# Kernel tuning notes

Hardware: AMD Instinct MI355X
Metric: run time of the kernel (lower is better)

Reference implementation:

```python
import jax, jax.numpy as jnp
import numpy as np

N, S, D, H = 4, 2048, 1024, 16
DH = D // H  # 64


def setup_inputs() -> dict:
    key = jax.random.key(0)
    ks = jax.random.split(key, 7)
    return {
        "sequences": jax.random.normal(ks[0], (N, S, D), dtype=jnp.float32),
        "Wq": jax.random.normal(ks[1], (H, DH, DH), dtype=jnp.float32) * (1.0 / np.sqrt(DH)),
        "bq": jax.random.normal(ks[2], (H, DH), dtype=jnp.float32) * 0.02,
        "Wk": jax.random.normal(ks[3], (H, DH, DH), dtype=jnp.float32) * (1.0 / np.sqrt(DH)),
        "bk": jax.random.normal(ks[4], (H, DH), dtype=jnp.float32) * 0.02,
        "Wv": jax.random.normal(ks[5], (H, DH, DH), dtype=jnp.float32) * (1.0 / np.sqrt(DH)),
        "bv": jax.random.normal(ks[6], (H, DH), dtype=jnp.float32) * 0.02,
    }


def reference(sequences, Wq, bq, Wk, bk, Wv, bv):
    n, s, d = sequences.shape
    # Each head h only sees its own slice of the embedding (block-diagonal proj)
    x = sequences.reshape(n, s, H, DH)  # (N, S, H, DH)
    q = jnp.einsum('nshd,hde->nshe', x, Wq) + bq  # (N, S, H, DH)
    k = jnp.einsum('nshd,hde->nshe', x, Wk) + bk
    v = jnp.einsum('nshd,hde->nshe', x, Wv) + bv
    scores = jnp.einsum('nqhd,nkhd->nhqk', q, k) / jnp.sqrt(jnp.float32(DH))
    attn = jax.nn.softmax(scores, axis=-1)  # (N, H, S, S)
    out = jnp.einsum('nhqk,nkhd->nqhd', attn, v)  # (N, S, H, DH)
    return out.reshape(n, s, d)  # hstack of heads == concat on last dim
```

## Files before the change

kernel.cpp:

```cpp
#include <hip/hip_runtime.h>
#include <hip/hip_bf16.h>

#define NB 4
#define SLEN 2048
#define DMODEL 1024
#define NH 16
#define DH 64

using f32x4  = __attribute__((ext_vector_type(4))) float;
using f32x8  = __attribute__((ext_vector_type(8))) float;
using f32x16 = __attribute__((ext_vector_type(16))) float;
using bf16x8 = __attribute__((ext_vector_type(8))) short;
using u32x4  = __attribute__((ext_vector_type(4))) unsigned int;

__device__ __forceinline__ unsigned short f2bf(float f) {
    unsigned int u = __float_as_uint(f);
    u += 0x7FFFu + ((u >> 16) & 1u);
    return (unsigned short)(u >> 16);
}

__device__ __forceinline__ float fast_exp2(float x) {
    float r;
    asm("v_exp_f32 %0, %1" : "=v"(r) : "v"(x));
    return r;
}

__device__ __forceinline__ unsigned cvtpk(float lo, float hi) {
    unsigned r;
    asm("v_cvt_pk_bf16_f32 %0, %1, %2" : "=v"(r) : "v"(lo), "v"(hi));
    return r;
}

__device__ __forceinline__ void permswap(unsigned& a, unsigned& b) {
    asm("v_permlane32_swap_b32 %0, %1" : "+v"(a), "+v"(b));
}

#define QSCALE 0.18033688011112042f

__global__ __launch_bounds__(256) void qkv_proj_kernel(
    const float* __restrict__ seq,
    const float* __restrict__ Wq, const float* __restrict__ bq,
    const float* __restrict__ Wk, const float* __restrict__ bk,
    const float* __restrict__ Wv, const float* __restrict__ bv,
    unsigned short* __restrict__ Qb,
    unsigned short* __restrict__ Kb,
    unsigned short* __restrict__ Vt)
{
    const int bid  = blockIdx.x;
    const int nh   = bid >> 5;
    const int tile = bid & 31;
    const int h = nh & 15;
    const int n = nh >> 4;
    const int t0 = tile * 64;
    const int tid = threadIdx.x;
    const int w  = tid >> 6;
    const int l  = tid & 63;
    const int g  = l >> 4;
    const int ln = l & 15;

    __shared__ unsigned short wt[3][64 * 72];

    {
        const float* Wsrc0 = Wq + h * 4096;
        const float* Wsrc1 = Wk + h * 4096;
        const float* Wsrc2 = Wv + h * 4096;
        for (int idx = tid; idx < 4096; idx += 256) {
            int d = idx >> 6, e = idx & 63;
            wt[0][e * 72 + d] = f2bf(Wsrc0[idx]);
            wt[1][e * 72 + d] = f2bf(Wsrc1[idx]);
            wt[2][e * 72 + d] = f2bf(Wsrc2[idx]);
        }
    }
    __syncthreads();

    const float* xrow = seq + ((size_t)(n * SLEN + t0 + w * 16 + ln)) * DMODEL + h * DH;
    bf16x8 a[2];
#pragma unroll
    for (int kk = 0; kk < 2; ++kk) {
        const float4* src = reinterpret_cast<const float4*>(xrow + kk * 32 + g * 8);
        float4 v0 = src[0];
        float4 v1 = src[1];
        bf16x8 av;
        av[0] = (short)f2bf(v0.x); av[1] = (short)f2bf(v0.y);
        av[2] = (short)f2bf(v0.z); av[3] = (short)f2bf(v0.w);
        av[4] = (short)f2bf(v1.x); av[5] = (short)f2bf(v1.y);
        av[6] = (short)f2bf(v1.z); av[7] = (short)f2bf(v1.w);
        a[kk] = av;
    }

    const float* bias0 = bq + h * DH;
    const float* bias1 = bk + h * DH;
    const float* bias2 = bv + h * DH;

#pragma unroll
    for (int p = 0; p < 3; ++p) {
#pragma unroll
        for (int cb = 0; cb < 4; ++cb) {
            f32x4 acc = {0.f, 0.f, 0.f, 0.f};
#pragma unroll
            for (int kk = 0; kk < 2; ++kk) {
                bf16x8 b = *reinterpret_cast<bf16x8*>(
                    &wt[p][(cb * 16 + ln) * 72 + kk * 32 + g * 8]);
                acc = __builtin_amdgcn_mfma_f32_16x16x32_bf16(a[kk], b, acc, 0, 0, 0);
            }
            const int col = cb * 16 + ln;
            if (p == 0) {
                const float bb = bias0[col];
#pragma unroll
                for (int r = 0; r < 4; ++r) {
                    float qv = (acc[r] + bb) * QSCALE;
                    Qb[((size_t)(nh * SLEN + t0 + w * 16 + g * 4 + r)) * DH + col] = f2bf(qv);
                }
            } else if (p == 1) {
                const float bb = bias1[col];
#pragma unroll
                for (int r = 0; r < 4; ++r) {
                    Kb[((size_t)(nh * SLEN + t0 + w * 16 + g * 4 + r)) * DH + col] =
                        f2bf(acc[r] + bb);
                }
            } else {
                const float bb = bias2[col];
                ushort4 pack;
                pack.x = f2bf(acc[0] + bb);
                pack.y = f2bf(acc[1] + bb);
                pack.z = f2bf(acc[2] + bb);
                pack.w = f2bf(acc[3] + bb);
                *reinterpret_cast<ushort4*>(
                    &Vt[((size_t)(nh * 64 + col)) * SLEN + t0 + w * 16 + g * 4]) = pack;
            }
        }
    }
}

__global__ __launch_bounds__(256) void attn_kernel(
    const unsigned short* __restrict__ Qb,
    const unsigned short* __restrict__ Kb,
    const unsigned short* __restrict__ Vt,
    float* __restrict__ out)
{
    const int bid = blockIdx.x;
    const int swz = (bid & 7) * 128 + (bid >> 3);
    const int nh = swz >> 4;
    const int qt = swz & 15;
    const int n = nh >> 4, h = nh & 15;
    const int tid = threadIdx.x;
    const int w  = tid >> 6;
    const int l  = tid & 63;
    const int lq = l & 31;
    const int hi = l >> 5;
    const int q0 = qt * 128 + w * 32;

    __shared__ unsigned short k_lds[2][64 * 64];
    __shared__ unsigned short v_lds[2][64 * 64];

    const int c_row = tid >> 3;
    const int c_sub = tid & 7;
    const int ws0 = ((c_sub ^ (c_row & 7) ^ (c_row >> 3)) & 7) * 8;
    const int wi0 = c_row * 64 + ws0;
    const int wi1 = (c_row + 32) * 64 + (ws0 ^ 32);

    const unsigned short* Kh = Kb + (size_t)nh * SLEN * DH;
    const unsigned short* Vh = Vt + (size_t)nh * DH * SLEN;
    const unsigned short* KgA = Kh + (size_t)c_row * DH + c_sub * 8;
    const unsigned short* KgB = KgA + (size_t)32 * DH;
    const unsigned short* VgA = Vh + (size_t)c_row * SLEN + c_sub * 8;
    const unsigned short* VgB = VgA + (size_t)32 * SLEN;

    const unsigned short* qrow = Qb + ((size_t)(nh * SLEN + q0 + lq)) * DH + hi * 8;
    bf16x8 qf[4];
#pragma unroll
    for (int ks = 0; ks < 4; ++ks)
        qf[ks] = *reinterpret_cast<const bf16x8*>(qrow + ks * 16);

    f32x16 oA, oB, zro;
    f32x8 lacc;
#pragma unroll
    for (int r = 0; r < 16; ++r) { oA[r] = 0.f; oB[r] = 0.f; zro[r] = 0.f; }
#pragma unroll
    for (int r = 0; r < 8; ++r) lacc[r] = 0.f;

    {
        bf16x8 kr0 = *reinterpret_cast<const bf16x8*>(KgA);
        bf16x8 kr1 = *reinterpret_cast<const bf16x8*>(KgB);
        bf16x8 vr0 = *reinterpret_cast<const bf16x8*>(VgA);
        bf16x8 vr1 = *reinterpret_cast<const bf16x8*>(VgB);
        *reinterpret_cast<bf16x8*>(&k_lds[0][wi0]) = kr0;
        *reinterpret_cast<bf16x8*>(&k_lds[0][wi1]) = kr1;
        *reinterpret_cast<bf16x8*>(&v_lds[0][wi0]) = vr0;
        *reinterpret_cast<bf16x8*>(&v_lds[0][wi1]) = vr1;
    }
    __syncthreads();

    const int rxg = (lq & 7) ^ (lq >> 3);
    int cur = 0;

    for (int kt = 0; kt < SLEN; kt += 64) {
        const int ktn = (kt + 64) & (SLEN - 1);

        bf16x8 kr0 = *reinterpret_cast<const bf16x8*>(KgA + (size_t)ktn * DH);
        bf16x8 kr1 = *reinterpret_cast<const bf16x8*>(KgB + (size_t)ktn * DH);
        bf16x8 vr0 = *reinterpret_cast<const bf16x8*>(VgA + ktn);
        bf16x8 vr1 = *reinterpret_cast<const bf16x8*>(VgB + ktn);

        const unsigned short* kb0 = &k_lds[cur][0];
        const unsigned short* vb0 = &v_lds[cur][0];

        f32x16 s0, s1;
        {
            bf16x8 kfA[4];
#pragma unroll
            for (int ks = 0; ks < 4; ++ks) {
                const int slot = (((ks * 2 + hi) ^ rxg) & 7) * 8;
                kfA[ks] = *reinterpret_cast<const bf16x8*>(&kb0[lq * 64 + slot]);
            }
            __builtin_amdgcn_s_setprio(1);
            s0 = __builtin_amdgcn_mfma_f32_32x32x16_bf16(kfA[0], qf[0], zro, 0, 0, 0);
#pragma unroll
            for (int ks = 1; ks < 4; ++ks)
                s0 = __builtin_amdgcn_mfma_f32_32x32x16_bf16(kfA[ks], qf[ks], s0, 0, 0, 0);
            __builtin_amdgcn_s_setprio(0);
        }
        {
            bf16x8 kfB[4];
#pragma unroll
            for (int ks = 0; ks < 4; ++ks) {
                const int slot = ((((ks * 2 + hi) ^ rxg) & 7) * 8) ^ 32;
                kfB[ks] = *reinterpret_cast<const bf16x8*>(&kb0[(lq + 32) * 64 + slot]);
            }
            __builtin_amdgcn_s_setprio(1);
            s1 = __builtin_amdgcn_mfma_f32_32x32x16_bf16(kfB[0], qf[0], zro, 0, 0, 0);
#pragma unroll
            for (int ks = 1; ks < 4; ++ks)
                s1 = __builtin_amdgcn_mfma_f32_32x32x16_bf16(kfB[ks], qf[ks], s1, 0, 0, 0);
            __builtin_amdgcn_s_setprio(0);
        }

#pragma unroll
        for (int r = 0; r < 16; ++r) {
            s0[r] = fast_exp2(s0[r]);
            s1[r] = fast_exp2(s1[r]);
        }
#pragma unroll
        for (int r = 0; r < 8; ++r)
            lacc[r] += (s0[r] + s0[r + 8]) + (s1[r] + s1[r + 8]);

        bf16x8 pa0[2], pa1[2];
#pragma unroll
        for (int f = 0; f < 2; ++f) {
            const int b = f * 8;
            unsigned a0 = cvtpk(s0[b + 0], s0[b + 1]);
            unsigned b0 = cvtpk(s0[b + 4], s0[b + 5]);
            permswap(a0, b0);
            unsigned a1 = cvtpk(s0[b + 2], s0[b + 3]);
            unsigned b1 = cvtpk(s0[b + 6], s0[b + 7]);
            permswap(a1, b1);
            u32x4 t0v = {a0, a1, b0, b1};
            pa0[f] = __builtin_bit_cast(bf16x8, t0v);

            unsigned c0 = cvtpk(s1[b + 0], s1[b + 1]);
            unsigned d0 = cvtpk(s1[b + 4], s1[b + 5]);
            permswap(c0, d0);
            unsigned c1 = cvtpk(s1[b + 2], s1[b + 3]);
            unsigned d1 = cvtpk(s1[b + 6], s1[b + 7]);
            permswap(c1, d1);
            u32x4 t1v = {c0, c1, d0, d1};
            pa1[f] = __builtin_bit_cast(bf16x8, t1v);
        }

        {
            bf16x8 vfA[4], vfB[4];
#pragma unroll
            for (int f = 0; f < 4; ++f) {
                const int slot = (((f * 2 + hi) ^ rxg) & 7) * 8;
                vfA[f] = *reinterpret_cast<const bf16x8*>(&vb0[lq * 64 + slot]);
                vfB[f] = *reinterpret_cast<const bf16x8*>(&vb0[(lq + 32) * 64 + (slot ^ 32)]);
            }
            __builtin_amdgcn_s_setprio(1);
#pragma unroll
            for (int f = 0; f < 2; ++f) {
                oA = __builtin_amdgcn_mfma_f32_32x32x16_bf16(vfA[f],     pa0[f], oA, 0, 0, 0);
                oB = __builtin_amdgcn_mfma_f32_32x32x16_bf16(vfB[f],     pa0[f], oB, 0, 0, 0);
                oA = __builtin_amdgcn_mfma_f32_32x32x16_bf16(vfA[f + 2], pa1[f], oA, 0, 0, 0);
                oB = __builtin_amdgcn_mfma_f32_32x32x16_bf16(vfB[f + 2], pa1[f], oB, 0, 0, 0);
            }
            __builtin_amdgcn_s_setprio(0);
        }

        if (ktn != 0) {
            *reinterpret_cast<bf16x8*>(&k_lds[cur ^ 1][wi0]) = kr0;
            *reinterpret_cast<bf16x8*>(&k_lds[cur ^ 1][wi1]) = kr1;
            *reinterpret_cast<bf16x8*>(&v_lds[cur ^ 1][wi0]) = vr0;
            *reinterpret_cast<bf16x8*>(&v_lds[cur ^ 1][wi1]) = vr1;
            __syncthreads();
            cur ^= 1;
        }
    }

    float lsum = ((lacc[0] + lacc[1]) + (lacc[2] + lacc[3]))
               + ((lacc[4] + lacc[5]) + (lacc[6] + lacc[7]));
    lsum += __shfl_xor(lsum, 32);

    const float inv = 1.0f / lsum;
    float* dst = out + ((size_t)(n * SLEN + q0 + lq)) * DMODEL + h * DH;
#pragma unroll
    for (int grp = 0; grp < 4; ++grp) {
        float4 stA, stB;
        stA.x = oA[4 * grp + 0] * inv; stA.y = oA[4 * grp + 1] * inv;
        stA.z = oA[4 * grp + 2] * inv; stA.w = oA[4 * grp + 3] * inv;
        stB.x = oB[4 * grp + 0] * inv; stB.y = oB[4 * grp + 1] * inv;
        stB.z = oB[4 * grp + 2] * inv; stB.w = oB[4 * grp + 3] * inv;
        *reinterpret_cast<float4*>(dst + grp * 8 + hi * 4)      = stA;
        *reinterpret_cast<float4*>(dst + 32 + grp * 8 + hi * 4) = stB;
    }
}

extern "C" void kernel_launch(void* const* d_in, const int* in_sizes, int n_in,
                              void* d_out, int out_size, void* d_ws, size_t ws_size,
                              hipStream_t stream) {
    const float* seq = (const float*)d_in[0];
    const float* Wq  = (const float*)d_in[1];
    const float* bq  = (const float*)d_in[2];
    const float* Wk  = (const float*)d_in[3];
    const float* bk  = (const float*)d_in[4];
    const float* Wv  = (const float*)d_in[5];
    const float* bv  = (const float*)d_in[6];

    const size_t per_tensor = (size_t)NB * NH * SLEN * DH;
    unsigned short* Qb = (unsigned short*)d_ws;
    unsigned short* Kb = Qb + per_tensor;
    unsigned short* Vt = Kb + per_tensor;

    qkv_proj_kernel<<<dim3(NB * NH * (SLEN / 64)), dim3(256), 0, stream>>>(
        seq, Wq, bq, Wk, bk, Wv, bv, Qb, Kb, Vt);
    attn_kernel<<<dim3(NB * NH * (SLEN / 128)), dim3(256), 0, stream>>>(
        Qb, Kb, Vt, (float*)d_out);
}
```

Before: 129.4 us.

## Double attention block to 512 threads sharing K/V tiles across eight waves

Attention blocks now cover 256 query rows with 8 waves instead of 128 rows with 4. Each K/V tile staged in LDS is reused by twice as many waves, and each thread issues one global load per tensor per tile instead of two. The key loop is unrolled by two with fixed ping-pong buffer pointers, which removes the runtime buffer index. In exchange, barriers synchronize more waves and the grid has half as many blocks, which can reduce latency hiding and occupancy balance.

```diff
diff --git a/kernel.cpp b/kernel.cpp
--- a/kernel.cpp
+++ b/kernel.cpp
@@ -132,39 +132,147 @@
     }
 }
 
-__global__ __launch_bounds__(256) void attn_kernel(
+struct AttnState {
+    const unsigned short* KgA;
+    const unsigned short* VgA;
+    int wi;
+    int lq, hi, rxg;
+};
+
+__device__ __forceinline__ void attn_iter(
+    const AttnState& st, int ktn,
+    const unsigned short* __restrict__ kb0, const unsigned short* __restrict__ vb0,
+    unsigned short* __restrict__ kbn, unsigned short* __restrict__ vbn,
+    const bf16x8 qf[4], f32x16& oA, f32x16& oB, f32x8& lacc, const f32x16& zro)
+{
+    const int lq = st.lq, hi = st.hi, rxg = st.rxg;
+
+    bf16x8 kr = *reinterpret_cast<const bf16x8*>(st.KgA + (size_t)ktn * DH);
+    bf16x8 vr = *reinterpret_cast<const bf16x8*>(st.VgA + ktn);
+
+    f32x16 s0, s1;
+    {
+        bf16x8 kfA[4];
+#pragma unroll
+        for (int ks = 0; ks < 4; ++ks) {
+            const int slot = (((ks * 2 + hi) ^ rxg) & 7) * 8;
+            kfA[ks] = *reinterpret_cast<const bf16x8*>(&kb0[lq * 64 + slot]);
+        }
+        __builtin_amdgcn_s_setprio(1);
+        s0 = __builtin_amdgcn_mfma_f32_32x32x16_bf16(kfA[0], qf[0], zro, 0, 0, 0);
+#pragma unroll
+        for (int ks = 1; ks < 4; ++ks)
+            s0 = __builtin_amdgcn_mfma_f32_32x32x16_bf16(kfA[ks], qf[ks], s0, 0, 0, 0);
+        __builtin_amdgcn_s_setprio(0);
+    }
+    {
+        bf16x8 kfB[4];
+#pragma unroll
+        for (int ks = 0; ks < 4; ++ks) {
+            const int slot = ((((ks * 2 + hi) ^ rxg) & 7) * 8) ^ 32;
+            kfB[ks] = *reinterpret_cast<const bf16x8*>(&kb0[(lq + 32) * 64 + slot]);
+        }
+        __builtin_amdgcn_s_setprio(1);
+        s1 = __builtin_amdgcn_mfma_f32_32x32x16_bf16(kfB[0], qf[0], zro, 0, 0, 0);
+#pragma unroll
+        for (int ks = 1; ks < 4; ++ks)
+            s1 = __builtin_amdgcn_mfma_f32_32x32x16_bf16(kfB[ks], qf[ks], s1, 0, 0, 0);
+        __builtin_amdgcn_s_setprio(0);
+    }
+
+#pragma unroll
+    for (int r = 0; r < 16; ++r) {
+        s0[r] = fast_exp2(s0[r]);
+        s1[r] = fast_exp2(s1[r]);
+    }
+#pragma unroll
+    for (int r = 0; r < 8; ++r)
+        lacc[r] += (s0[r] + s0[r + 8]) + (s1[r] + s1[r + 8]);
+
+    bf16x8 pa0[2], pa1[2];
+#pragma unroll
+    for (int f = 0; f < 2; ++f) {
+        const int b = f * 8;
+        unsigned a0 = cvtpk(s0[b + 0], s0[b + 1]);
+        unsigned b0 = cvtpk(s0[b + 4], s0[b + 5]);
+        permswap(a0, b0);
+        unsigned a1 = cvtpk(s0[b + 2], s0[b + 3]);
+        unsigned b1 = cvtpk(s0[b + 6], s0[b + 7]);
+        permswap(a1, b1);
+        u32x4 t0v = {a0, a1, b0, b1};
+        pa0[f] = __builtin_bit_cast(bf16x8, t0v);
+
+        unsigned c0 = cvtpk(s1[b + 0], s1[b + 1]);
+        unsigned d0 = cvtpk(s1[b + 4], s1[b + 5]);
+        permswap(c0, d0);
+        unsigned c1 = cvtpk(s1[b + 2], s1[b + 3]);
+        unsigned d1 = cvtpk(s1[b + 6], s1[b + 7]);
+        permswap(c1, d1);
+        u32x4 t1v = {c0, c1, d0, d1};
+        pa1[f] = __builtin_bit_cast(bf16x8, t1v);
+    }
+
+    {
+        bf16x8 vfA[4], vfB[4];
+#pragma unroll
+        for (int f = 0; f < 4; ++f) {
+            const int slot = (((f * 2 + hi) ^ rxg) & 7) * 8;
+            vfA[f] = *reinterpret_cast<const bf16x8*>(&vb0[lq * 64 + slot]);
+            vfB[f] = *reinterpret_cast<const bf16x8*>(&vb0[(lq + 32) * 64 + (slot ^ 32)]);
+        }
+        __builtin_amdgcn_s_setprio(1);
+#pragma unroll
+        for (int f = 0; f < 2; ++f) {
+            oA = __builtin_amdgcn_mfma_f32_32x32x16_bf16(vfA[f],     pa0[f], oA, 0, 0, 0);
+            oB = __builtin_amdgcn_mfma_f32_32x32x16_bf16(vfB[f],     pa0[f], oB, 0, 0, 0);
+            oA = __builtin_amdgcn_mfma_f32_32x32x16_bf16(vfA[f + 2], pa1[f], oA, 0, 0, 0);
+            oB = __builtin_amdgcn_mfma_f32_32x32x16_bf16(vfB[f + 2], pa1[f], oB, 0, 0, 0);
+        }
+        __builtin_amdgcn_s_setprio(0);
+    }
+
+    if (ktn != 0) {
+        *reinterpret_cast<bf16x8*>(&kbn[st.wi]) = kr;
+        *reinterpret_cast<bf16x8*>(&vbn[st.wi]) = vr;
+        __syncthreads();
+    }
+}
+
+__global__ __launch_bounds__(512) void attn_kernel(
     const unsigned short* __restrict__ Qb,
     const unsigned short* __restrict__ Kb,
     const unsigned short* __restrict__ Vt,
     float* __restrict__ out)
 {
     const int bid = blockIdx.x;
-    const int swz = (bid & 7) * 128 + (bid >> 3);
-    const int nh = swz >> 4;
-    const int qt = swz & 15;
+    const int swz = (bid & 7) * 64 + (bid >> 3);
+    const int nh = swz >> 3;
+    const int qt = swz & 7;
     const int n = nh >> 4, h = nh & 15;
     const int tid = threadIdx.x;
     const int w  = tid >> 6;
     const int l  = tid & 63;
     const int lq = l & 31;
     const int hi = l >> 5;
-    const int q0 = qt * 128 + w * 32;
+    const int q0 = qt * 256 + w * 32;
 
     __shared__ unsigned short k_lds[2][64 * 64];
     __shared__ unsigned short v_lds[2][64 * 64];
 
     const int c_row = tid >> 3;
     const int c_sub = tid & 7;
-    const int ws0 = ((c_sub ^ (c_row & 7) ^ (c_row >> 3)) & 7) * 8;
-    const int wi0 = c_row * 64 + ws0;
-    const int wi1 = (c_row + 32) * 64 + (ws0 ^ 32);
+    const int slot0 = (c_sub ^ (c_row & 7) ^ ((c_row >> 3) & 7)) & 7;
+    const int wi = c_row * 64 + slot0 * 8;
 
     const unsigned short* Kh = Kb + (size_t)nh * SLEN * DH;
     const unsigned short* Vh = Vt + (size_t)nh * DH * SLEN;
-    const unsigned short* KgA = Kh + (size_t)c_row * DH + c_sub * 8;
-    const unsigned short* KgB = KgA + (size_t)32 * DH;
-    const unsigned short* VgA = Vh + (size_t)c_row * SLEN + c_sub * 8;
-    const unsigned short* VgB = VgA + (size_t)32 * SLEN;
+
+    AttnState st;
+    st.KgA = Kh + (size_t)c_row * DH + c_sub * 8;
+    st.VgA = Vh + (size_t)c_row * SLEN + c_sub * 8;
+    st.wi = wi;
+    st.lq = lq; st.hi = hi;
+    st.rxg = (lq & 7) ^ (lq >> 3);
 
     const unsigned short* qrow = Qb + ((size_t)(nh * SLEN + q0 + lq)) * DH + hi * 8;
     bf16x8 qf[4];
@@ -180,120 +288,18 @@
     for (int r = 0; r < 8; ++r) lacc[r] = 0.f;
 
     {
-        bf16x8 kr0 = *reinterpret_cast<const bf16x8*>(KgA);
-        bf16x8 kr1 = *reinterpret_cast<const bf16x8*>(KgB);
-        bf16x8 vr0 = *reinterpret_cast<const bf16x8*>(VgA);
-        bf16x8 vr1 = *reinterpret_cast<const bf16x8*>(VgB);
-        *reinterpret_cast<bf16x8*>(&k_lds[0][wi0]) = kr0;
-        *reinterpret_cast<bf16x8*>(&k_lds[0][wi1]) = kr1;
-        *reinterpret_cast<bf16x8*>(&v_lds[0][wi0]) = vr0;
-        *reinterpret_cast<bf16x8*>(&v_lds[0][wi1]) = vr1;
+        bf16x8 kr = *reinterpret_cast<const bf16x8*>(st.KgA);
+        bf16x8 vr = *reinterpret_cast<const bf16x8*>(st.VgA);
+        *reinterpret_cast<bf16x8*>(&k_lds[0][wi]) = kr;
+        *reinterpret_cast<bf16x8*>(&v_lds[0][wi]) = vr;
     }
     __syncthreads();
 
-    const int rxg = (lq & 7) ^ (lq >> 3);
-    int cur = 0;
-
-    for (int kt = 0; kt < SLEN; kt += 64) {
-        const int ktn = (kt + 64) & (SLEN - 1);
-
-        bf16x8 kr0 = *reinterpret_cast<const bf16x8*>(KgA + (size_t)ktn * DH);
-        bf16x8 kr1 = *reinterpret_cast<const bf16x8*>(KgB + (size_t)ktn * DH);
-        bf16x8 vr0 = *reinterpret_cast<const bf16x8*>(VgA + ktn);
-        bf16x8 vr1 = *reinterpret_cast<const bf16x8*>(VgB + ktn);
-
-        const unsigned short* kb0 = &k_lds[cur][0];
-        const unsigned short* vb0 = &v_lds[cur][0];
-
-        f32x16 s0, s1;
-        {
-            bf16x8 kfA[4];
-#pragma unroll
-            for (int ks = 0; ks < 4; ++ks) {
-                const int slot = (((ks * 2 + hi) ^ rxg) & 7) * 8;
-                kfA[ks] = *reinterpret_cast<const bf16x8*>(&kb0[lq * 64 + slot]);
-            }
-            __builtin_amdgcn_s_setprio(1);
-            s0 = __builtin_amdgcn_mfma_f32_32x32x16_bf16(kfA[0], qf[0], zro, 0, 0, 0);
-#pragma unroll
-            for (int ks = 1; ks < 4; ++ks)
-                s0 = __builtin_amdgcn_mfma_f32_32x32x16_bf16(kfA[ks], qf[ks], s0, 0, 0, 0);
-            __builtin_amdgcn_s_setprio(0);
-        }
-        {
-            bf16x8 kfB[4];
-#pragma unroll
-            for (int ks = 0; ks < 4; ++ks) {
-                const int slot = ((((ks * 2 + hi) ^ rxg) & 7) * 8) ^ 32;
-                kfB[ks] = *reinterpret_cast<const bf16x8*>(&kb0[(lq + 32) * 64 + slot]);
-            }
-            __builtin_amdgcn_s_setprio(1);
-            s1 = __builtin_amdgcn_mfma_f32_32x32x16_bf16(kfB[0], qf[0], zro, 0, 0, 0);
-#pragma unroll
-            for (int ks = 1; ks < 4; ++ks)
-                s1 = __builtin_amdgcn_mfma_f32_32x32x16_bf16(kfB[ks], qf[ks], s1, 0, 0, 0);
-            __builtin_amdgcn_s_setprio(0);
-        }
-
-#pragma unroll
-        for (int r = 0; r < 16; ++r) {
-            s0[r] = fast_exp2(s0[r]);
-            s1[r] = fast_exp2(s1[r]);
-        }
-#pragma unroll
-        for (int r = 0; r < 8; ++r)
-            lacc[r] += (s0[r] + s0[r + 8]) + (s1[r] + s1[r + 8]);
-
-        bf16x8 pa0[2], pa1[2];
-#pragma unroll
-        for (int f = 0; f < 2; ++f) {
-            const int b = f * 8;
-            unsigned a0 = cvtpk(s0[b + 0], s0[b + 1]);
-            unsigned b0 = cvtpk(s0[b + 4], s0[b + 5]);
-            permswap(a0, b0);
-            unsigned a1 = cvtpk(s0[b + 2], s0[b + 3]);
-            unsigned b1 = cvtpk(s0[b + 6], s0[b + 7]);
-            permswap(a1, b1);
-            u32x4 t0v = {a0, a1, b0, b1};
-            pa0[f] = __builtin_bit_cast(bf16x8, t0v);
-
-            unsigned c0 = cvtpk(s1[b + 0], s1[b + 1]);
-            unsigned d0 = cvtpk(s1[b + 4], s1[b + 5]);
-            permswap(c0, d0);
-            unsigned c1 = cvtpk(s1[b + 2], s1[b + 3]);
-            unsigned d1 = cvtpk(s1[b + 6], s1[b + 7]);
-            permswap(c1, d1);
-            u32x4 t1v = {c0, c1, d0, d1};
-            pa1[f] = __builtin_bit_cast(bf16x8, t1v);
-        }
-
-        {
-            bf16x8 vfA[4], vfB[4];
-#pragma unroll
-            for (int f = 0; f < 4; ++f) {
-                const int slot = (((f * 2 + hi) ^ rxg) & 7) * 8;
-                vfA[f] = *reinterpret_cast<const bf16x8*>(&vb0[lq * 64 + slot]);
-                vfB[f] = *reinterpret_cast<const bf16x8*>(&vb0[(lq + 32) * 64 + (slot ^ 32)]);
-            }
-            __builtin_amdgcn_s_setprio(1);
-#pragma unroll
-            for (int f = 0; f < 2; ++f) {
-                oA = __builtin_amdgcn_mfma_f32_32x32x16_bf16(vfA[f],     pa0[f], oA, 0, 0, 0);
-                oB = __builtin_amdgcn_mfma_f32_32x32x16_bf16(vfB[f],     pa0[f], oB, 0, 0, 0);
-                oA = __builtin_amdgcn_mfma_f32_32x32x16_bf16(vfA[f + 2], pa1[f], oA, 0, 0, 0);
-                oB = __builtin_amdgcn_mfma_f32_32x32x16_bf16(vfB[f + 2], pa1[f], oB, 0, 0, 0);
-            }
-            __builtin_amdgcn_s_setprio(0);
-        }
-
-        if (ktn != 0) {
-            *reinterpret_cast<bf16x8*>(&k_lds[cur ^ 1][wi0]) = kr0;
-            *reinterpret_cast<bf16x8*>(&k_lds[cur ^ 1][wi1]) = kr1;
-            *reinterpret_cast<bf16x8*>(&v_lds[cur ^ 1][wi0]) = vr0;
-            *reinterpret_cast<bf16x8*>(&v_lds[cur ^ 1][wi1]) = vr1;
-            __syncthreads();
-            cur ^= 1;
-        }
+    for (int kt = 0; kt < SLEN; kt += 128) {
+        attn_iter(st, kt + 64, &k_lds[0][0], &v_lds[0][0],
+                  &k_lds[1][0], &v_lds[1][0], qf, oA, oB, lacc, zro);
+        attn_iter(st, (kt + 128) & (SLEN - 1), &k_lds[1][0], &v_lds[1][0],
+                  &k_lds[0][0], &v_lds[0][0], qf, oA, oB, lacc, zro);
     }
 
     float lsum = ((lacc[0] + lacc[1]) + (lacc[2] + lacc[3]))
@@ -332,6 +338,6 @@
 
     qkv_proj_kernel<<<dim3(NB * NH * (SLEN / 64)), dim3(256), 0, stream>>>(
         seq, Wq, bq, Wk, bk, Wv, bv, Qb, Kb, Vt);
-    attn_kernel<<<dim3(NB * NH * (SLEN / 128)), dim3(256), 0, stream>>>(
+    attn_kernel<<<dim3(NB * NH * (SLEN / 256)), dim3(512), 0, stream>>>(
         Qb, Kb, Vt, (float*)d_out);
 }
```

Measured after the change: 106.8 us. 17.5% less time.
